# Kernel tuning notes

Hardware: AMD Instinct MI355X
Metric: run time of the kernel (lower is better)

The kernel has to match this reference:

```python
import jax, jax.numpy as jnp
import numpy as np


def conv1d(x, w, b):
    # x: [B, Cin, L], w: [Cout, Cin, K] (torch layout), padding=1
    out = jax.lax.conv_general_dilated(
        x, w, window_strides=(1,), padding=[(1, 1)],
        dimension_numbers=('NCH', 'OIH', 'NCH'))
    return out + b[None, :, None]


def maxpool2(x):
    # MaxPool1d(kernel=2, stride=2) on last dim
    return jax.lax.reduce_window(x, -jnp.inf, jax.lax.max,
                                 (1, 1, 2), (1, 1, 2), 'VALID')


def build_edges(B, n):
    # bidirectional chain edges per graph + self-loops (GCNConv default)
    base = (jnp.arange(B) * n)[:, None]          # [B,1]
    i = jnp.arange(n - 1)[None, :]               # [1,n-1]
    s = (base + i).reshape(-1)
    d = s + 1
    loop = jnp.arange(B * n)
    src = jnp.concatenate([s, d, loop])
    dst = jnp.concatenate([d, s, loop])
    return src, dst


def gcn_conv(x, w, b, src, dst, deg_isqrt, n_total):
    # PyG GCNConv: X' = D^-1/2 (A+I) D^-1/2 (X W) + b
    h = x @ w                                    # [N, Dout]
    norm = deg_isqrt[src] * deg_isqrt[dst]       # [E]
    agg = jax.ops.segment_sum(h[src] * norm[:, None], dst,
                              num_segments=n_total)
    return agg + b


def setup_inputs() -> dict:
    key = jax.random.key(0)
    ks = jax.random.split(key, 12)
    B, L = 64, 16384
    CF, H, NC = 8, 64, 2
    sd = lambda fan_in: 1.0 / np.sqrt(fan_in)
    return {
        'x': jax.random.normal(ks[0], (B, 1, L), jnp.float32),
        'batch_size': B,
        'conv1_w': jax.random.normal(ks[1], (CF, 1, 3), jnp.float32) * sd(3),
        'conv1_b': jax.random.normal(ks[2], (CF,), jnp.float32) * 0.01,
        'conv2_w': jax.random.normal(ks[3], (CF, CF, 3), jnp.float32) * sd(3 * CF),
        'conv2_b': jax.random.normal(ks[4], (CF,), jnp.float32) * 0.01,
        'gcn1_w': jax.random.normal(ks[5], (CF, H), jnp.float32) * sd(CF),
        'gcn1_b': jax.random.normal(ks[6], (H,), jnp.float32) * 0.01,
        'gcn2_w': jax.random.normal(ks[7], (H, H), jnp.float32) * sd(H),
        'gcn2_b': jax.random.normal(ks[8], (H,), jnp.float32) * 0.01,
        'fc_w': jax.random.normal(ks[9], (H, NC), jnp.float32) * sd(H),
        'fc_b': jax.random.normal(ks[10], (NC,), jnp.float32) * 0.01,
    }


def reference(x, batch_size, conv1_w, conv1_b, conv2_w, conv2_b,
              gcn1_w, gcn1_b, gcn2_w, gcn2_b, fc_w, fc_b):
    # CNN feature extractor
    h = maxpool2(jax.nn.relu(conv1d(x, conv1_w, conv1_b)))
    h = maxpool2(jax.nn.relu(conv1d(h, conv2_w, conv2_b)))
    h = jnp.transpose(h, (0, 2, 1))              # [B, n, CF]
    B, n, C = h.shape
    N = B * n
    nodes = h.reshape(N, C)
    # line-graph message passing (GCNConv x2), dropout is identity at eval
    src, dst = build_edges(B, n)
    deg = jax.ops.segment_sum(jnp.ones_like(dst, jnp.float32), dst,
                              num_segments=N)
    deg_isqrt = jax.lax.rsqrt(deg)
    h1 = jax.nn.relu(gcn_conv(nodes, gcn1_w, gcn1_b, src, dst, deg_isqrt, N))
    h2 = jax.nn.relu(gcn_conv(h1, gcn2_w, gcn2_b, src, dst, deg_isqrt, N))
    # global_mean_pool: nodes are contiguous per graph
    pooled = h2.reshape(B, n, -1).mean(axis=1)   # [B, H]
    return pooled @ fc_w + fc_b                  # [B, num_classes]
```

## Files before the change

### kernel.cpp

```cpp
#include <hip/hip_runtime.h>
#include <hip/hip_fp16.h>

typedef _Float16 half8 __attribute__((ext_vector_type(8)));
typedef __attribute__((ext_vector_type(4))) float f32x4;

#define BATCH 64
#define L0 16384
#define L1 8192
#define NPG 4096
#define CF 8
#define H 64
#define CHUNK 128
#define NCHUNK 32
#define NCHUNKS_TOTAL 2048

#define A_T1   0
#define P_W1T  11008
#define P_WCT  15104
#define A_H1   0
#define A_ND   18720
#define A_RED  20832
#define A_W2T  21856
#define ARENA_BYTES 30048

__device__ __forceinline__ float disv(int p) {
    if (p < 0 || p >= NPG) return 0.f;
    if (p == 0 || p == NPG - 1) return 0.70710678118654752f;
    return 0.57735026918962576f;
}
__device__ __forceinline__ unsigned packh2(float a, float b) {
    union { __half2 h; unsigned u; } cv;
    cv.h = __float22half2_rn(make_float2(a, b));
    return cv.u;
}
__device__ __forceinline__ unsigned short h1u(float f) {
    union { __half h; unsigned short u; } cv;
    cv.h = __float2half_rn(f);
    return cv.u;
}
__device__ __forceinline__ unsigned pkadd3(unsigned a, unsigned b, unsigned c) {
    union { unsigned u; __half2 h; } A, B, C, R;
    A.u = a; B.u = b; C.u = c;
    R.h = __hadd2(__hadd2(A.h, B.h), C.h);
    return R.u;
}
__device__ __forceinline__ float2 uph2(unsigned u) {
    union { unsigned uu; __half2 h; } cv; cv.uu = u;
    return __half22float2(cv.h);
}

__global__ __launch_bounds__(256, 5) void k_fused(const float* __restrict__ x,
        const float* __restrict__ c1w, const float* __restrict__ c1b,
        const float* __restrict__ c2w, const float* __restrict__ c2b,
        const float* __restrict__ g1w, const float* __restrict__ g1b,
        const float* __restrict__ g2w, const float* __restrict__ g2b,
        float* __restrict__ partials) {
    __shared__ __align__(16) char arena[ARENA_BYTES];
    unsigned short* t1_l = (unsigned short*)(arena + A_T1);
    unsigned short* nd_l = (unsigned short*)(arena + A_ND);
    unsigned short* h1_l = (unsigned short*)(arena + A_H1);
    unsigned short* w2t  = (unsigned short*)(arena + A_W2T);
    unsigned short* w1t  = (unsigned short*)(arena + P_W1T);
    unsigned short* wct  = (unsigned short*)(arena + P_WCT);
    float*          red  = (float*)(arena + A_RED);
    unsigned* w2t32 = (unsigned*)w2t;
    unsigned* w1t32 = (unsigned*)w1t;

    const int tid = threadIdx.x;
    const int wave = tid >> 6;
    const int l = tid & 63;
    const int m = l & 15, q = l >> 4;
    const float T = 1.f / 3.f;
    const f32x4 z4 = {0.f, 0.f, 0.f, 0.f};

    const int chunk = blockIdx.x;
    const int b = chunk >> 5, ch = chunk & 31;
    const int s = ch * CHUNK;
    const bool edgeblk = (ch == 0) || (ch == NCHUNK - 1);

    {
        uint4 z = {0u, 0u, 0u, 0u};
        *(uint4*)&w1t[tid * 8] = z;
        if (tid < 64) *(uint4*)&wct[tid * 8] = z;
    }
    __syncthreads();

    #pragma unroll
    for (int j = 0; j < 8; ++j) {
        int p = tid + 256 * j;
        int n = p & 63, rest = p >> 6;
        int i2 = rest & 3, qq = (rest >> 2) & 3, ks = rest >> 4;
        int e0 = (ks * 32 + qq * 8 + 2 * i2) * 64 + n;
        int lane = qq * 16 + (n & 15), ct = n >> 4;
        w2t32[((ct * 2 + ks) * 64 + lane) * 4 + i2] =
            packh2(g2w[e0] * T, g2w[e0 + 64] * T);
    }
    {
        int n = tid & 63, i2 = tid >> 6;
        int e0 = (2 * i2) * 64 + n;
        w1t32[((n >> 4) * 64 + (n & 15)) * 4 + i2] =
            packh2(g1w[e0] * T, g1w[e0 + 64] * T);
    }
    if (tid < 192) {
        int co = tid / 24, rem2 = tid % 24, ci = rem2 / 3, tap = rem2 % 3;
        wct[(tap * 16 + co) * 8 + ci] = h1u(c2w[tid]);
    }
    {
        const float* xb = x + (size_t)b * L0;
        float wA[8], wB[8], wC[8], bb[8];
        #pragma unroll
        for (int c = 0; c < 8; ++c) {
            wA[c] = c1w[3 * c]; wB[c] = c1w[3 * c + 1]; wC[c] = c1w[3 * c + 2];
            bb[c] = c1b[c];
        }
        #pragma unroll
        for (int it2 = 0; it2 < 2; ++it2) {
            int t = tid + it2 * 256;
            if (t < 266) {
                uint4 o = {0u, 0u, 0u, 0u};
                int g = 2 * s - 5 + t;
                if (g >= 0 && g < L1) {
                    int col = 2 * g - 1;
                    float a0 = (col >= 0) ? xb[col] : 0.f;
                    float a1 = xb[col + 1];
                    float a2 = xb[col + 2];
                    float a3 = (col + 3 < L0) ? xb[col + 3] : 0.f;
                    unsigned pw[4];
                    #pragma unroll
                    for (int c = 0; c < 4; ++c) {
                        int c0 = 2 * c, c1_ = 2 * c + 1;
                        float y00 = bb[c0] + wA[c0] * a0 + wB[c0] * a1 + wC[c0] * a2;
                        float y01 = bb[c0] + wA[c0] * a1 + wB[c0] * a2 + wC[c0] * a3;
                        float y10 = bb[c1_] + wA[c1_] * a0 + wB[c1_] * a1 + wC[c1_] * a2;
                        float y11 = bb[c1_] + wA[c1_] * a1 + wB[c1_] * a2 + wC[c1_] * a3;
                        pw[c] = packh2(fmaxf(fmaxf(y00, y01), 0.f),
                                       fmaxf(fmaxf(y10, y11), 0.f));
                    }
                    o.x = pw[0]; o.y = pw[1]; o.z = pw[2]; o.w = pw[3];
                }
                *(uint4*)&t1_l[t * 8] = o;
            }
        }
    }
    __syncthreads();

    half8 w1fr[4];
    {
        half8 wcfr = ((const half8*)wct)[l];
        float bb2 = (m < CF) ? c2b[m] : 0.f;
        auto convC = [&](int rt) {
            int rr = rt * 16 + m + q;
            rr = rr > 265 ? 265 : rr;
            half8 a = *(const half8*)&t1_l[rr * 8];
            f32x4 c = __builtin_amdgcn_mfma_f32_16x16x32_f16(a, wcfr, z4, 0, 0, 0);
            if (m < CF) {
                int n0 = rt * 8 + q * 2;
                if (n0 < 132)
                    nd_l[n0 * 8 + m] = h1u(fmaxf(fmaxf(c[0], c[1]) + bb2, 0.f));
                if (n0 + 1 < 132)
                    nd_l[(n0 + 1) * 8 + m] = h1u(fmaxf(fmaxf(c[2], c[3]) + bb2, 0.f));
            }
        };
        convC(wave); convC(wave + 4); convC(wave + 8); convC(wave + 12);
        if (wave == 0) convC(16);
        #pragma unroll
        for (int ct = 0; ct < 4; ++ct)
            w1fr[ct] = ((const half8*)w1t)[ct * 64 + l];
    }
    __syncthreads();

    {
        float4 b1v[4];
        #pragma unroll
        for (int ct = 0; ct < 4; ++ct)
            b1v[ct] = *(const float4*)&g1b[ct * 16 + q * 4];
        auto doD = [&](int rt) {
            int rc = rt * 16 + m;
            int rcc = rc > 129 ? 129 : rc;
            uint4 RL = *(const uint4*)&nd_l[rcc * 8];
            uint4 RM = *(const uint4*)&nd_l[(rcc + 1) * 8];
            uint4 RH = *(const uint4*)&nd_l[(rcc + 2) * 8];
            union { unsigned u[4]; half8 h8; } sf;
            if (!edgeblk) {
                sf.u[0] = pkadd3(RL.x, RM.x, RH.x);
                sf.u[1] = pkadd3(RL.y, RM.y, RH.y);
                sf.u[2] = pkadd3(RL.z, RM.z, RH.z);
                sf.u[3] = pkadd3(RL.w, RM.w, RH.w);
            } else {
                int p = s - 1 + rcc;
                float dc = disv(p);
                float cm_ = 3.f * dc * dc;
                float cl_ = 3.f * dc * disv(p - 1);
                float cr_ = 3.f * dc * disv(p + 1);
                #define SFE(e, UL, UM, UH)                                    \
                  { float2 Lf = uph2(UL), Mf = uph2(UM), Hf = uph2(UH);       \
                    sf.u[e] = packh2(cm_*Mf.x + cl_*Lf.x + cr_*Hf.x,          \
                                     cm_*Mf.y + cl_*Lf.y + cr_*Hf.y); }
                SFE(0, RL.x, RM.x, RH.x)
                SFE(1, RL.y, RM.y, RH.y)
                SFE(2, RL.z, RM.z, RH.z)
                SFE(3, RL.w, RM.w, RH.w)
                #undef SFE
            }
            bool wok = rc < 130;
            #pragma unroll
            for (int ct = 0; ct < 4; ++ct) {
                f32x4 c = __builtin_amdgcn_mfma_f32_16x16x32_f16(
                    w1fr[ct], sf.h8, z4, 0, 0, 0);
                if (wok) {
                    unsigned p01 = packh2(fmaxf(c[0] + b1v[ct].x, 0.f),
                                          fmaxf(c[1] + b1v[ct].y, 0.f));
                    unsigned p23 = packh2(fmaxf(c[2] + b1v[ct].z, 0.f),
                                          fmaxf(c[3] + b1v[ct].w, 0.f));
                    *(uint2*)&h1_l[rc * 72 + ct * 16 + q * 4] =
                        make_uint2(p01, p23);
                }
            }
        };
        doD(wave); doD(wave + 4);
        if (wave == 0) doD(8);
    }
    __syncthreads();

    {
        half8 w2fr[4][2];
        float b2v[4];
        #pragma unroll
        for (int ct = 0; ct < 4; ++ct) {
            w2fr[ct][0] = ((const half8*)w2t)[(ct * 2 + 0) * 64 + l];
            w2fr[ct][1] = ((const half8*)w2t)[(ct * 2 + 1) * 64 + l];
            b2v[ct] = g2b[ct * 16 + m];
        }
        float pool_acc[4] = {0.f, 0.f, 0.f, 0.f};
        auto doE = [&](int rt) {
            f32x4 accg[4] = {z4, z4, z4, z4};
            int r0 = rt * 16 + m;
            float cl_ = 0.f, cm_ = 0.f, cr_ = 0.f;
            if (edgeblk) {
                int p = s + r0;
                float dcp = disv(p);
                cm_ = 3.f * dcp * dcp;
                cl_ = 3.f * dcp * disv(p - 1);
                cr_ = 3.f * dcp * disv(p + 1);
            }
            #pragma unroll
            for (int ks = 0; ks < 2; ++ks) {
                int koff = ks * 32 + q * 8;
                uint4 lo = *(const uint4*)&h1_l[r0 * 72 + koff];
                uint4 mi = *(const uint4*)&h1_l[(r0 + 1) * 72 + koff];
                uint4 hi = *(const uint4*)&h1_l[(r0 + 2) * 72 + koff];
                union { unsigned u[4]; half8 h8; } a2;
                if (!edgeblk) {
                    a2.u[0] = pkadd3(lo.x, mi.x, hi.x);
                    a2.u[1] = pkadd3(lo.y, mi.y, hi.y);
                    a2.u[2] = pkadd3(lo.z, mi.z, hi.z);
                    a2.u[3] = pkadd3(lo.w, mi.w, hi.w);
                } else {
                    #define A2E(e, UL, UM, UH)                                \
                      { float2 Lf = uph2(UL), Mf = uph2(UM), Hf = uph2(UH);   \
                        a2.u[e] = packh2(cm_*Mf.x + cl_*Lf.x + cr_*Hf.x,      \
                                         cm_*Mf.y + cl_*Lf.y + cr_*Hf.y); }
                    A2E(0, lo.x, mi.x, hi.x)
                    A2E(1, lo.y, mi.y, hi.y)
                    A2E(2, lo.z, mi.z, hi.z)
                    A2E(3, lo.w, mi.w, hi.w)
                    #undef A2E
                }
                #pragma unroll
                for (int ct = 0; ct < 4; ++ct)
                    accg[ct] = __builtin_amdgcn_mfma_f32_16x16x32_f16(
                        a2.h8, w2fr[ct][ks], accg[ct], 0, 0, 0);
            }
            #pragma unroll
            for (int ct = 0; ct < 4; ++ct)
                #pragma unroll
                for (int i = 0; i < 4; ++i)
                    pool_acc[ct] += fmaxf(accg[ct][i] + b2v[ct], 0.f);
        };
        doE(wave); doE(wave + 4);
        #pragma unroll
        for (int ct = 0; ct < 4; ++ct) {
            float v = pool_acc[ct];
            v += __shfl_xor(v, 16);
            v += __shfl_xor(v, 32);
            if (q == 0) red[wave * 64 + ct * 16 + m] = v;
        }
    }
    __syncthreads();
    if (tid < H) {
        partials[(size_t)chunk * H + tid] = red[tid] + red[64 + tid]
                                          + red[128 + tid] + red[192 + tid];
    }
}

__global__ __launch_bounds__(256) void k_final(const float* __restrict__ partials,
        const float* __restrict__ fcw, const float* __restrict__ fcb,
        float* __restrict__ out) {
    __shared__ float red[4][H];
    __shared__ float pool_l[H];
    int bgr = blockIdx.x;
    int tid = threadIdx.x;
    int g = tid >> 6, j = tid & 63;
    float acc = 0.f;
    for (int c = g; c < NCHUNK; c += 4)
        acc += partials[((size_t)bgr * NCHUNK + c) * H + j];
    red[g][j] = acc;
    __syncthreads();
    if (tid < H)
        pool_l[j] = (red[0][j] + red[1][j] + red[2][j] + red[3][j]) * (1.f / NPG);
    __syncthreads();
    if (tid < 2) {
        float o = fcb[tid];
        for (int k = 0; k < H; ++k) o += pool_l[k] * fcw[k * 2 + tid];
        out[bgr * 2 + tid] = o;
    }
}

extern "C" void kernel_launch(void* const* d_in, const int* in_sizes, int n_in,
                              void* d_out, int out_size, void* d_ws, size_t ws_size,
                              hipStream_t stream) {
    (void)in_sizes; (void)n_in; (void)out_size; (void)ws_size;
    const float* x   = (const float*)d_in[0];
    const float* c1w = (const float*)d_in[2];
    const float* c1b = (const float*)d_in[3];
    const float* c2w = (const float*)d_in[4];
    const float* c2b = (const float*)d_in[5];
    const float* g1w = (const float*)d_in[6];
    const float* g1b = (const float*)d_in[7];
    const float* g2w = (const float*)d_in[8];
    const float* g2b = (const float*)d_in[9];
    const float* fcw = (const float*)d_in[10];
    const float* fcb = (const float*)d_in[11];
    float* out = (float*)d_out;

    float* partials = (float*)d_ws;

    k_fused<<<NCHUNKS_TOTAL, 256, 0, stream>>>(x, c1w, c1b, c2w, c2b,
                                               g1w, g1b, g2w, g2b, partials);
    k_final<<<BATCH, 256, 0, stream>>>(partials, fcw, fcb, out);
}
```

Before: 24.89 us.

## Fuse final pooling and FC into main kernel via last-block atomic counter

Removes the separate k_final launch. Each block now atomically bumps a per-graph counter after writing its partial sums, and the last block of each graph reduces the partials and applies the FC layer. This trades a kernel launch and its dependency gap for a memset launch, an atomic per block and an extra barrier. The memory ordering relies on the acquire-release atomic making the other blocks' partial writes visible.

After: 56.20 us. 2.26x slower.

```diff
diff --git a/kernel.cpp b/kernel.cpp
--- a/kernel.cpp
+++ b/kernel.cpp
@@ -54,8 +54,11 @@
         const float* __restrict__ c2w, const float* __restrict__ c2b,
         const float* __restrict__ g1w, const float* __restrict__ g1b,
         const float* __restrict__ g2w, const float* __restrict__ g2b,
-        float* __restrict__ partials) {
+        const float* __restrict__ fcw, const float* __restrict__ fcb,
+        float* __restrict__ partials, unsigned* __restrict__ cnt,
+        float* __restrict__ out) {
     __shared__ __align__(16) char arena[ARENA_BYTES];
+    __shared__ unsigned lastf;
     unsigned short* t1_l = (unsigned short*)(arena + A_T1);
     unsigned short* nd_l = (unsigned short*)(arena + A_ND);
     unsigned short* h1_l = (unsigned short*)(arena + A_H1);
@@ -291,28 +294,35 @@
         partials[(size_t)chunk * H + tid] = red[tid] + red[64 + tid]
                                           + red[128 + tid] + red[192 + tid];
     }
-}
-
-__global__ __launch_bounds__(256) void k_final(const float* __restrict__ partials,
-        const float* __restrict__ fcw, const float* __restrict__ fcb,
-        float* __restrict__ out) {
-    __shared__ float red[4][H];
-    __shared__ float pool_l[H];
-    int bgr = blockIdx.x;
-    int tid = threadIdx.x;
-    int g = tid >> 6, j = tid & 63;
-    float acc = 0.f;
-    for (int c = g; c < NCHUNK; c += 4)
-        acc += partials[((size_t)bgr * NCHUNK + c) * H + j];
-    red[g][j] = acc;
-    __syncthreads();
-    if (tid < H)
-        pool_l[j] = (red[0][j] + red[1][j] + red[2][j] + red[3][j]) * (1.f / NPG);
-    __syncthreads();
-    if (tid < 2) {
-        float o = fcb[tid];
-        for (int k = 0; k < H; ++k) o += pool_l[k] * fcw[k * 2 + tid];
-        out[bgr * 2 + tid] = o;
+    __syncthreads();
+
+    if (tid == 0) {
+        unsigned old = __hip_atomic_fetch_add(&cnt[b], 1u, __ATOMIC_ACQ_REL,
+                                              __HIP_MEMORY_SCOPE_AGENT);
+        lastf = (old == NCHUNK - 1) ? 1u : 0u;
+    }
+    __syncthreads();
+    if (lastf) {
+        float acc = 0.f;
+        for (int c = wave; c < NCHUNK; c += 4)
+            acc += partials[((size_t)b * NCHUNK + c) * H + l];
+        red[wave * 64 + l] = acc;
+        __syncthreads();
+        if (tid < H) {
+            float v = (red[tid] + red[64 + tid] + red[128 + tid] + red[192 + tid])
+                      * (1.f / NPG);
+            float s0 = v * fcw[tid * 2 + 0];
+            float s1 = v * fcw[tid * 2 + 1];
+            #pragma unroll
+            for (int o = 32; o; o >>= 1) {
+                s0 += __shfl_down(s0, o);
+                s1 += __shfl_down(s1, o);
+            }
+            if (tid == 0) {
+                out[b * 2 + 0] = s0 + fcb[0];
+                out[b * 2 + 1] = s1 + fcb[1];
+            }
+        }
     }
 }
 
@@ -334,8 +344,10 @@
     float* out = (float*)d_out;
 
     float* partials = (float*)d_ws;
-
+    unsigned* cnt = (unsigned*)(partials + (size_t)NCHUNKS_TOTAL * H);
+
+    hipMemsetAsync(cnt, 0, BATCH * sizeof(unsigned), stream);
     k_fused<<<NCHUNKS_TOTAL, 256, 0, stream>>>(x, c1w, c1b, c2w, c2b,
-                                               g1w, g1b, g2w, g2b, partials);
-    k_final<<<BATCH, 256, 0, stream>>>(partials, fcw, fcb, out);
-}
+                                               g1w, g1b, g2w, g2b, fcw, fcb,
+                                               partials, cnt, out);
+}
```
